# Kernel optimization log

Hardware: AMD Instinct MI355X
Metric: run time of the kernel (lower is better)

## Reference

```python
import jax, jax.numpy as jnp
import numpy as np

NUM_NODES = 10000
NUM_EDGES = 8192
NNZ = 320000
TOP_K = 5


def setup_inputs() -> dict:
    key = jax.random.key(0)
    k1, k2 = jax.random.split(key)
    # incidence list: row 0 = node ids (V_idx), row 1 = hyperedge ids (E_idx)
    edge_index = jax.random.randint(k1, (2, NNZ), 0, NUM_EDGES, dtype=jnp.int32).astype(jnp.int64)
    logits = jax.random.normal(k2, (NUM_NODES, NUM_EDGES), dtype=jnp.float32)
    return {"edge_index": edge_index, "logits": logits}


def reference(edge_index, logits):
    # Deterministic (is_test=True) path of NeuralSparseHG.forward.
    V_idx = edge_index[0]
    E_idx = edge_index[1]
    scores = jax.nn.sigmoid(logits[V_idx, E_idx])  # [nnz]

    nnz = V_idx.shape[0]
    num_nodes = logits.shape[0]

    # Segmented top-k: sort incidences by (node, -score); within each node's
    # contiguous group the first TOP_K entries are kept. This replaces the
    # original per-node Python loop with one parallel sort + rank pass.
    order = jnp.lexsort((-scores, V_idx))           # primary key V_idx asc, secondary score desc
    sorted_v = V_idx[order]
    group_start = jnp.searchsorted(sorted_v, jnp.arange(num_nodes))  # [num_nodes]
    rank_in_group = jnp.arange(nnz) - group_start[sorted_v]
    keep_sorted = rank_in_group < TOP_K

    hard_mask = jnp.zeros(nnz, scores.dtype).at[order].set(keep_sorted.astype(scores.dtype))
    # straight-through estimator (value == hard_mask, gradient == d scores)
    soft_mask = jax.lax.stop_gradient(hard_mask - scores) + scores
    keep_mask = soft_mask > 0

    # JAX cannot return data-dependent shapes under jit: instead of compacting
    # to [2, n_keep], dropped incidences are masked to -1 (same information).
    pruned_edge_index = jnp.where(keep_mask[None, :], edge_index, -1)
    return pruned_edge_index, scores
```

## Files before the change

kernel.cpp:

```cpp
#include <hip/hip_runtime.h>

#define NUM_NODES 10000
#define TOP_K 5
#define CAP 128

__global__ void k_zero(int* __restrict__ p, int n) {
    int i = blockIdx.x * blockDim.x + threadIdx.x;
    if (i < n) p[i] = 0;
}

__global__ void k_score(const int* __restrict__ edge,
                        const float* __restrict__ logits,
                        float* __restrict__ out,
                        int* __restrict__ cnt,
                        unsigned long long* __restrict__ bucket,
                        int nnz, int num_edges) {
    int i = blockIdx.x * blockDim.x + threadIdx.x;
    if (i >= nnz) return;
    int v = edge[i];
    int e = edge[nnz + i];
    float x = logits[(long long)v * num_edges + e];
    float s = 1.0f / (1.0f + expf(-x));
    out[i]           = -1.0f;
    out[nnz + i]     = -1.0f;
    out[2 * nnz + i] = s;
    unsigned long long key =
        ((unsigned long long)__float_as_uint(s) << 32) |
        (unsigned int)(0xFFFFFFFFu - (unsigned int)i);
    int pos = atomicAdd(&cnt[v], 1);
    if (pos < CAP) bucket[(long long)pos * NUM_NODES + v] = key;
}

__global__ void k_topk(const int* __restrict__ edge,
                       const int* __restrict__ cnt,
                       const unsigned long long* __restrict__ bucket,
                       float* __restrict__ out, int nnz) {
    int v = blockIdx.x * blockDim.x + threadIdx.x;
    if (v >= NUM_NODES) return;
    int n = cnt[v];
    if (n > CAP) n = CAP;
    if (n <= 0) return;

    unsigned long long b0 = 0, b1 = 0, b2 = 0, b3 = 0, b4 = 0;
    for (int p = 0; p < n; p++) {
        unsigned long long k = bucket[(long long)p * NUM_NODES + v];
        unsigned long long t;
        t = (k > b0) ? k : b0;  k = (k > b0) ? b0 : k;  b0 = t;
        t = (k > b1) ? k : b1;  k = (k > b1) ? b1 : k;  b1 = t;
        t = (k > b2) ? k : b2;  k = (k > b2) ? b2 : k;  b2 = t;
        t = (k > b3) ? k : b3;  k = (k > b3) ? b3 : k;  b3 = t;
        b4 = (k > b4) ? k : b4;
    }

    int m = (n < TOP_K) ? n : TOP_K;
    #define EMIT(bj, j)                                                        \
        if (m > (j)) {                                                         \
            int i = (int)(0xFFFFFFFFu - (unsigned int)((bj) & 0xFFFFFFFFu));   \
            out[i]       = (float)v;                                           \
            out[nnz + i] = (float)edge[nnz + i];                               \
        }
    EMIT(b0, 0) EMIT(b1, 1) EMIT(b2, 2) EMIT(b3, 3) EMIT(b4, 4)
    #undef EMIT
}

extern "C" void kernel_launch(void* const* d_in, const int* in_sizes, int n_in,
                              void* d_out, int out_size, void* d_ws, size_t ws_size,
                              hipStream_t stream) {
    const int*   edge   = (const int*)d_in[0];
    const float* logits = (const float*)d_in[1];
    float*       out    = (float*)d_out;
    int nnz       = in_sizes[0] / 2;
    int num_edges = in_sizes[1] / NUM_NODES;

    unsigned long long* bucket = (unsigned long long*)d_ws;
    int* cnt = (int*)(bucket + (size_t)CAP * NUM_NODES);

    k_zero <<<(NUM_NODES + 255) / 256, 256, 0, stream>>>(cnt, NUM_NODES);
    k_score<<<(nnz + 255) / 256,       256, 0, stream>>>(edge, logits, out, cnt, bucket, nnz, num_edges);
    k_topk <<<(NUM_NODES + 255) / 256, 256, 0, stream>>>(edge, cnt, bucket, out, nnz);
}
```

Baseline: 409.4 us.

## Use one wavefront per node for top-k with node-major buckets and packed edge ids

The top-k stage now assigns a 64-lane wavefront to each node instead of a single thread. Each lane loads up to two keys from a contiguous node-major bucket, and the top five are found by repeated shuffle-xor max reductions. The key now packs the edge id into its low bits, so the extra global read of edge ids at emit time goes away, and a memset replaces the zeroing kernel. The packing assumes index and edge counts fit in 19 and 13 bits. Scattered bucket writes in the scoring kernel may become less coalesced.

```diff
diff --git a/kernel.cpp b/kernel.cpp
--- a/kernel.cpp
+++ b/kernel.cpp
@@ -3,11 +3,6 @@
 #define NUM_NODES 10000
 #define TOP_K 5
 #define CAP 128
-
-__global__ void k_zero(int* __restrict__ p, int n) {
-    int i = blockIdx.x * blockDim.x + threadIdx.x;
-    if (i < n) p[i] = 0;
-}
 
 __global__ void k_score(const int* __restrict__ edge,
                         const float* __restrict__ logits,
@@ -26,41 +21,45 @@
     out[2 * nnz + i] = s;
     unsigned long long key =
         ((unsigned long long)__float_as_uint(s) << 32) |
-        (unsigned int)(0xFFFFFFFFu - (unsigned int)i);
+        ((unsigned long long)(0x7FFFFu - (unsigned int)i) << 13) |
+        (unsigned long long)(unsigned int)e;
     int pos = atomicAdd(&cnt[v], 1);
-    if (pos < CAP) bucket[(long long)pos * NUM_NODES + v] = key;
+    if (pos < CAP) bucket[(long long)v * CAP + pos] = key;
 }
 
-__global__ void k_topk(const int* __restrict__ edge,
-                       const int* __restrict__ cnt,
+__global__ void k_topk(const int* __restrict__ cnt,
                        const unsigned long long* __restrict__ bucket,
                        float* __restrict__ out, int nnz) {
-    int v = blockIdx.x * blockDim.x + threadIdx.x;
+    int wave = threadIdx.x >> 6;
+    int lane = threadIdx.x & 63;
+    int v = blockIdx.x * 4 + wave;
     if (v >= NUM_NODES) return;
     int n = cnt[v];
     if (n > CAP) n = CAP;
     if (n <= 0) return;
 
-    unsigned long long b0 = 0, b1 = 0, b2 = 0, b3 = 0, b4 = 0;
-    for (int p = 0; p < n; p++) {
-        unsigned long long k = bucket[(long long)p * NUM_NODES + v];
-        unsigned long long t;
-        t = (k > b0) ? k : b0;  k = (k > b0) ? b0 : k;  b0 = t;
-        t = (k > b1) ? k : b1;  k = (k > b1) ? b1 : k;  b1 = t;
-        t = (k > b2) ? k : b2;  k = (k > b2) ? b2 : k;  b2 = t;
-        t = (k > b3) ? k : b3;  k = (k > b3) ? b3 : k;  b3 = t;
-        b4 = (k > b4) ? k : b4;
+    const unsigned long long* b = bucket + (long long)v * CAP;
+    unsigned long long k0 = (lane      < n) ? b[lane]      : 0ull;
+    unsigned long long k1 = (lane + 64 < n) ? b[lane + 64] : 0ull;
+
+    #pragma unroll
+    for (int t = 0; t < TOP_K; t++) {
+        unsigned long long m = (k0 > k1) ? k0 : k1;
+        #pragma unroll
+        for (int d = 32; d >= 1; d >>= 1) {
+            unsigned long long o = __shfl_xor(m, d, 64);
+            m = (o > m) ? o : m;
+        }
+        if (m == 0ull) break;
+        k0 = (k0 == m) ? 0ull : k0;
+        k1 = (k1 == m) ? 0ull : k1;
+        if (lane == 0) {
+            int e = (int)(m & 0x1FFFull);
+            int i = 0x7FFFF - (int)((m >> 13) & 0x7FFFFull);
+            out[i]       = (float)v;
+            out[nnz + i] = (float)e;
+        }
     }
-
-    int m = (n < TOP_K) ? n : TOP_K;
-    #define EMIT(bj, j)                                                        \
-        if (m > (j)) {                                                         \
-            int i = (int)(0xFFFFFFFFu - (unsigned int)((bj) & 0xFFFFFFFFu));   \
-            out[i]       = (float)v;                                           \
-            out[nnz + i] = (float)edge[nnz + i];                               \
-        }
-    EMIT(b0, 0) EMIT(b1, 1) EMIT(b2, 2) EMIT(b3, 3) EMIT(b4, 4)
-    #undef EMIT
 }
 
 extern "C" void kernel_launch(void* const* d_in, const int* in_sizes, int n_in,
@@ -73,9 +72,9 @@
     int num_edges = in_sizes[1] / NUM_NODES;
 
     unsigned long long* bucket = (unsigned long long*)d_ws;
-    int* cnt = (int*)(bucket + (size_t)CAP * NUM_NODES);
+    int* cnt = (int*)(bucket + (size_t)NUM_NODES * CAP);
 
-    k_zero <<<(NUM_NODES + 255) / 256, 256, 0, stream>>>(cnt, NUM_NODES);
-    k_score<<<(nnz + 255) / 256,       256, 0, stream>>>(edge, logits, out, cnt, bucket, nnz, num_edges);
-    k_topk <<<(NUM_NODES + 255) / 256, 256, 0, stream>>>(edge, cnt, bucket, out, nnz);
+    hipMemsetAsync(cnt, 0, NUM_NODES * sizeof(int), stream);
+    k_score<<<(nnz + 255) / 256,      256, 0, stream>>>(edge, logits, out, cnt, bucket, nnz, num_edges);
+    k_topk <<<(NUM_NODES + 3) / 4,    256, 0, stream>>>(cnt, bucket, out, nnz);
 }
```

Result: faster. 387.3 us (-5.4%).
